# Performance work log

Hardware: AMD Instinct MI355X
Metric: run time of the kernel (lower is better)

Reference implementation:

```python
import jax, jax.numpy as jnp
import numpy as np


def setup_inputs() -> dict:
    key = jax.random.key(0)
    ks = jax.random.split(key, 7)
    B, T, E, H = 4, 4096, 1024, 64
    return {
        "idx": jax.random.normal(ks[0], (B, T, E), dtype=jnp.float32),
        "Wq": jax.random.normal(ks[1], (E, H), dtype=jnp.float32) * (E ** -0.5),
        "bq": jax.random.normal(ks[2], (H,), dtype=jnp.float32) * 0.01,
        "Wk": jax.random.normal(ks[3], (E, H), dtype=jnp.float32) * (E ** -0.5),
        "bk": jax.random.normal(ks[4], (H,), dtype=jnp.float32) * 0.01,
        "Wv": jax.random.normal(ks[5], (E, H), dtype=jnp.float32) * (E ** -0.5),
        "bv": jax.random.normal(ks[6], (H,), dtype=jnp.float32) * 0.01,
    }


def reference(idx, Wq, bq, Wk, bk, Wv, bv):
    # idx: [B, T, E]
    d = idx.shape[-1]  # note: torch code scales by n_embd**-0.5, NOT head_size
    Q = idx @ Wq + bq  # [B, T, H]
    K = idx @ Wk + bk
    V = idx @ Wv + bv
    # scores; NOTE: original torch code calls wei.masked_fill(...) non-in-place
    # and discards the result, so no causal mask is applied. No softmax either.
    wei = jnp.einsum("bth,bsh->bts", Q, K) * (d ** -0.5)  # [B, T, T]
    out = jnp.einsum("bts,bsh->bth", wei, V)  # [B, T, H]
    return out
```

## Files before the change

kernel.cpp:

```cpp
#include <hip/hip_runtime.h>


typedef __attribute__((ext_vector_type(8))) short bf16x8;
typedef __attribute__((ext_vector_type(4))) float f32x4;

#define MFMA16(a, b, c) __builtin_amdgcn_mfma_f32_16x16x32_bf16((a), (b), (c), 0, 0, 0)

__device__ __forceinline__ unsigned short f2bf(float f) {
    unsigned int u = __float_as_uint(f);
    u += 0x7fffu + ((u >> 16) & 1u);
    return (unsigned short)(u >> 16);
}

__global__ void prep(const float* __restrict__ Wq, const float* __restrict__ Wk,
                     const float* __restrict__ Wv, unsigned short* __restrict__ WB) {
    int t = blockIdx.x * 256 + threadIdx.x;
    int kki = t / 768;
    int rem = t - kki * 768;
    int nt = rem >> 6, lane = rem & 63;
    int n = nt * 16 + (lane & 15);
    int kb = kki * 32 + ((lane >> 4) * 8);
    int mm = n >> 6, h = n & 63;
    const float* W = (mm == 0) ? Wq : (mm == 1) ? Wk : Wv;
    float sc = (mm == 1) ? 0.03125f : 1.0f;
    bf16x8 v;
    #pragma unroll
    for (int j = 0; j < 8; j++) v[j] = (short)f2bf(W[(size_t)(kb + j) * 64 + h] * sc);
    *(bf16x8*)(WB + (size_t)t * 8) = v;
}

__global__ __launch_bounds__(256, 4) void qkv(
    const float* __restrict__ idx, const unsigned short* __restrict__ WB,
    const float* __restrict__ bq, const float* __restrict__ bk, const float* __restrict__ bv,
    unsigned short* __restrict__ Q, unsigned short* __restrict__ Kt,
    unsigned short* __restrict__ Vt) {
    __shared__ unsigned short As[16 * 1032];
    const int lane = threadIdx.x & 63, w = threadIdx.x >> 6;
    const int r0 = blockIdx.x * 16;

    const float* src = idx + (size_t)(r0 + w * 4) * 1024;
    #pragma unroll
    for (int batch = 0; batch < 2; batch++) {
        float4 v[8];
        #pragma unroll
        for (int j = 0; j < 8; j++)
            v[j] = *(const float4*)(src + (size_t)(batch * 8 + j) * 256 + lane * 4);
        #pragma unroll
        for (int j = 0; j < 8; j++) {
            int i   = batch * 8 + j;
            int row = w * 4 + (i >> 2);
            int k   = (i & 3) * 256 + lane * 4;
            unsigned int lo = ((unsigned int)f2bf(v[j].y) << 16) | f2bf(v[j].x);
            unsigned int hi = ((unsigned int)f2bf(v[j].w) << 16) | f2bf(v[j].z);
            uint2 p; p.x = lo; p.y = hi;
            *(uint2*)(As + (size_t)row * 1032 + k) = p;
        }
    }
    __syncthreads();

    const f32x4 z4 = {0.f, 0.f, 0.f, 0.f};
    f32x4 acc[3] = {z4, z4, z4};

    const unsigned short* a_base = As + (size_t)(lane & 15) * 1032 + ((lane >> 4) * 8);
    bf16x8 a_c = *(const bf16x8*)(a_base);
    bf16x8 bc[3], bn[3];
    {
        const unsigned short* Bp = WB + (size_t)(lane * 8);
        #pragma unroll
        for (int j = 0; j < 3; j++) bc[j] = *(const bf16x8*)(Bp + (w + j * 4) * 512);
    }
    for (int kk = 0; kk < 32; kk++) {
        bf16x8 a_n = a_c;
        if (kk < 31) {
            const unsigned short* Bp = WB + (size_t)(((kk + 1) * 12) * 64 + lane) * 8;
            #pragma unroll
            for (int j = 0; j < 3; j++) bn[j] = *(const bf16x8*)(Bp + (w + j * 4) * 512);
            a_n = *(const bf16x8*)(a_base + (kk + 1) * 32);
        }
        #pragma unroll
        for (int j = 0; j < 3; j++) acc[j] = MFMA16(a_c, bc[j], acc[j]);
        #pragma unroll
        for (int j = 0; j < 3; j++) bc[j] = bn[j];
        a_c = a_n;
    }

    __syncthreads();
    unsigned short* Lq = As;
    unsigned short* Lk = As + 1024;
    unsigned short* Lv = As + 2048;
    const int h   = w * 16 + (lane & 15);
    const int row = (lane >> 4) * 4;
    {
        float bias0 = bq[h], bias1 = bk[h] * 0.03125f, bias2 = bv[h];
        #pragma unroll
        for (int reg = 0; reg < 4; reg++) {
            int r = row + reg;
            Lq[r * 64 + h] = f2bf(acc[0][reg] + bias0);
            Lk[h * 16 + r] = f2bf(acc[1][reg] + bias1);
            Lv[h * 16 + r] = f2bf(acc[2][reg] + bias2);
        }
    }
    __syncthreads();
    {
        const int tt = threadIdx.x;
        int qr = tt >> 4, qh = (tt & 15) * 4;
        *(uint2*)(Q + (size_t)(r0 + qr) * 64 + qh) = *(const uint2*)(Lq + qr * 64 + qh);
        int b = r0 >> 12, t0 = r0 & 4095;
        int hh = tt >> 2, tc = (tt & 3) * 4;
        *(uint2*)(Kt + (size_t)b * 262144 + hh * 4096 + t0 + tc) =
            *(const uint2*)(Lk + hh * 16 + tc);
        *(uint2*)(Vt + (size_t)b * 262144 + hh * 4096 + t0 + tc) =
            *(const uint2*)(Lv + hh * 16 + tc);
    }
}

__global__ __launch_bounds__(256) void ktv_partial(
    const unsigned short* __restrict__ Kt, const unsigned short* __restrict__ Vt,
    float* __restrict__ part) {
    const int lane = threadIdx.x & 63, wave = threadIdx.x >> 6;
    const int c = blockIdx.x, b = blockIdx.y;
    const unsigned short* Kb = Kt + (size_t)b * 262144;
    const unsigned short* Vb = Vt + (size_t)b * 262144;
    const f32x4 z4 = {0.f, 0.f, 0.f, 0.f};
    f32x4 acc[4] = {z4, z4, z4, z4};
    const int m  = 16 * wave + (lane & 15);
    const int tq = (lane >> 4) * 8;
    #pragma unroll
    for (int it = 0; it < 4; it++) {
        int t0 = c * 128 + it * 32 + tq;
        bf16x8 a = *(const bf16x8*)&Kb[(size_t)m * 4096 + t0];
        #pragma unroll
        for (int nt = 0; nt < 4; nt++) {
            bf16x8 bb = *(const bf16x8*)&Vb[(size_t)(nt * 16 + (lane & 15)) * 4096 + t0];
            acc[nt] = MFMA16(a, bb, acc[nt]);
        }
    }
    float* P = part + (size_t)(b * 32 + c) * 4096;
    const int rowb = 16 * wave + (lane >> 4) * 4;
    #pragma unroll
    for (int nt = 0; nt < 4; nt++)
        #pragma unroll
        for (int reg = 0; reg < 4; reg++)
            P[(rowb + reg) * 64 + nt * 16 + (lane & 15)] = acc[nt][reg];
}

__global__ void reduce_m(const float* __restrict__ part,
                         unsigned short* __restrict__ Mt) {
    int i = blockIdx.x * 256 + threadIdx.x;
    int b = i >> 12, h1 = (i >> 6) & 63, h2 = i & 63;
    float s = 0.f;
    #pragma unroll
    for (int cc = 0; cc < 32; cc++)
        s += part[(size_t)(b * 32 + cc) * 4096 + h1 * 64 + h2];
    Mt[(size_t)b * 4096 + h2 * 64 + h1] = f2bf(s);
}

__global__ __launch_bounds__(256) void qm(
    const unsigned short* __restrict__ Q, const unsigned short* __restrict__ Mt,
    float* __restrict__ out) {
    const int lane = threadIdx.x & 63, wave = threadIdx.x >> 6;
    const int r0 = blockIdx.x * 64;
    const int b  = r0 >> 12;
    const f32x4 z4 = {0.f, 0.f, 0.f, 0.f};
    f32x4 acc[4] = {z4, z4, z4, z4};
    const int rr = r0 + 16 * wave + (lane & 15);
    const int kq = (lane >> 4) * 8;
    #pragma unroll
    for (int ks = 0; ks < 2; ks++) {
        int k0 = ks * 32;
        bf16x8 a = *(const bf16x8*)&Q[(size_t)rr * 64 + k0 + kq];
        #pragma unroll
        for (int nt = 0; nt < 4; nt++) {
            bf16x8 bb = *(const bf16x8*)&Mt[(size_t)b * 4096 + (nt * 16 + (lane & 15)) * 64 + k0 + kq];
            acc[nt] = MFMA16(a, bb, acc[nt]);
        }
    }
    const int rowb = r0 + 16 * wave + (lane >> 4) * 4;
    #pragma unroll
    for (int nt = 0; nt < 4; nt++)
        #pragma unroll
        for (int reg = 0; reg < 4; reg++)
            out[(size_t)(rowb + reg) * 64 + nt * 16 + (lane & 15)] = acc[nt][reg];
}

extern "C" void kernel_launch(void* const* d_in, const int* in_sizes, int n_in,
                              void* d_out, int out_size, void* d_ws, size_t ws_size,
                              hipStream_t stream) {
    const float* idx = (const float*)d_in[0];
    const float* Wq  = (const float*)d_in[1];
    const float* bq  = (const float*)d_in[2];
    const float* Wk  = (const float*)d_in[3];
    const float* bk  = (const float*)d_in[4];
    const float* Wv  = (const float*)d_in[5];
    const float* bv  = (const float*)d_in[6];
    float* out = (float*)d_out;

    char* ws = (char*)d_ws;
    unsigned short* WB = (unsigned short*)(ws);
    float*          Pp = (float*)(ws);
    unsigned short* Q  = (unsigned short*)(ws + (2048u << 10));
    unsigned short* Kt = (unsigned short*)(ws + (4096u << 10));
    unsigned short* Vt = (unsigned short*)(ws + (6144u << 10));
    unsigned short* Mt = (unsigned short*)(ws + (8192u << 10));

    hipLaunchKernelGGL(prep,        dim3(96),     dim3(256), 0, stream, Wq, Wk, Wv, WB);
    hipLaunchKernelGGL(qkv,         dim3(1024),   dim3(256), 0, stream,
                       idx, WB, bq, bk, bv, Q, Kt, Vt);
    hipLaunchKernelGGL(ktv_partial, dim3(32, 4),  dim3(256), 0, stream, Kt, Vt, Pp);
    hipLaunchKernelGGL(reduce_m,    dim3(64),     dim3(256), 0, stream, Pp, Mt);
    hipLaunchKernelGGL(qm,          dim3(256),    dim3(256), 0, stream, Q, Mt, out);
}
```

Baseline: 125.9 us.

## Double rows per QKV block and fold K^T V reduction into atomics

The QKV projection block now handles 32 rows instead of 16, so each weight fragment loaded from global memory feeds two MFMAs. The B prefetch is also deepened to two steps ahead, and the Q/K/V stores are widened to 16 bytes. The separate reduce kernel is removed: ktv atomically adds its partials into a float M zeroed by prep, and qm converts and transposes M into LDS itself. This saves one launch and the partial-buffer traffic, at the cost of lower occupancy in qkv and atomic contention on the shared M.

```diff
diff --git a/kernel.cpp b/kernel.cpp
--- a/kernel.cpp
+++ b/kernel.cpp
@@ -13,8 +13,10 @@
 }
 
 __global__ void prep(const float* __restrict__ Wq, const float* __restrict__ Wk,
-                     const float* __restrict__ Wv, unsigned short* __restrict__ WB) {
+                     const float* __restrict__ Wv, unsigned short* __restrict__ WB,
+                     float* __restrict__ Mf) {
     int t = blockIdx.x * 256 + threadIdx.x;
+    if (t < 16384) Mf[t] = 0.f;
     int kki = t / 768;
     int rem = t - kki * 768;
     int nt = rem >> 6, lane = rem & 63;
@@ -29,18 +31,18 @@
     *(bf16x8*)(WB + (size_t)t * 8) = v;
 }
 
-__global__ __launch_bounds__(256, 4) void qkv(
+__global__ __launch_bounds__(256, 2) void qkv(
     const float* __restrict__ idx, const unsigned short* __restrict__ WB,
     const float* __restrict__ bq, const float* __restrict__ bk, const float* __restrict__ bv,
     unsigned short* __restrict__ Q, unsigned short* __restrict__ Kt,
     unsigned short* __restrict__ Vt) {
-    __shared__ unsigned short As[16 * 1032];
+    __shared__ unsigned short As[32 * 1032];
     const int lane = threadIdx.x & 63, w = threadIdx.x >> 6;
-    const int r0 = blockIdx.x * 16;
-
-    const float* src = idx + (size_t)(r0 + w * 4) * 1024;
-    #pragma unroll
-    for (int batch = 0; batch < 2; batch++) {
+    const int r0 = blockIdx.x * 32;
+
+    const float* src = idx + (size_t)(r0 + w * 8) * 1024;
+    #pragma unroll
+    for (int batch = 0; batch < 4; batch++) {
         float4 v[8];
         #pragma unroll
         for (int j = 0; j < 8; j++)
@@ -48,7 +50,7 @@
         #pragma unroll
         for (int j = 0; j < 8; j++) {
             int i   = batch * 8 + j;
-            int row = w * 4 + (i >> 2);
+            int row = w * 8 + (i >> 2);
             int k   = (i & 3) * 256 + lane * 4;
             unsigned int lo = ((unsigned int)f2bf(v[j].y) << 16) | f2bf(v[j].x);
             unsigned int hi = ((unsigned int)f2bf(v[j].w) << 16) | f2bf(v[j].z);
@@ -59,64 +61,80 @@
     __syncthreads();
 
     const f32x4 z4 = {0.f, 0.f, 0.f, 0.f};
-    f32x4 acc[3] = {z4, z4, z4};
-
-    const unsigned short* a_base = As + (size_t)(lane & 15) * 1032 + ((lane >> 4) * 8);
-    bf16x8 a_c = *(const bf16x8*)(a_base);
-    bf16x8 bc[3], bn[3];
-    {
-        const unsigned short* Bp = WB + (size_t)(lane * 8);
-        #pragma unroll
-        for (int j = 0; j < 3; j++) bc[j] = *(const bf16x8*)(Bp + (w + j * 4) * 512);
+    f32x4 acc[2][3] = {{z4, z4, z4}, {z4, z4, z4}};
+
+    const unsigned short* a_base0 = As + (size_t)(lane & 15) * 1032 + ((lane >> 4) * 8);
+    const unsigned short* a_base1 = a_base0 + 16 * 1032;
+    bf16x8 a_c[2], b0[3], b1[3], b2[3];
+    a_c[0] = *(const bf16x8*)a_base0;
+    a_c[1] = *(const bf16x8*)a_base1;
+    {
+        const unsigned short* Bp0 = WB + (size_t)(lane * 8);
+        const unsigned short* Bp1 = WB + (size_t)(12 * 64 + lane) * 8;
+        #pragma unroll
+        for (int j = 0; j < 3; j++) {
+            b0[j] = *(const bf16x8*)(Bp0 + (w + j * 4) * 512);
+            b1[j] = *(const bf16x8*)(Bp1 + (w + j * 4) * 512);
+            b2[j] = b1[j];
+        }
     }
     for (int kk = 0; kk < 32; kk++) {
-        bf16x8 a_n = a_c;
+        bf16x8 na0 = a_c[0], na1 = a_c[1];
+        if (kk < 30) {
+            const unsigned short* Bp = WB + (size_t)(((kk + 2) * 12) * 64 + lane) * 8;
+            #pragma unroll
+            for (int j = 0; j < 3; j++) b2[j] = *(const bf16x8*)(Bp + (w + j * 4) * 512);
+        }
         if (kk < 31) {
-            const unsigned short* Bp = WB + (size_t)(((kk + 1) * 12) * 64 + lane) * 8;
+            na0 = *(const bf16x8*)(a_base0 + (kk + 1) * 32);
+            na1 = *(const bf16x8*)(a_base1 + (kk + 1) * 32);
+        }
+        #pragma unroll
+        for (int j = 0; j < 3; j++) {
+            acc[0][j] = MFMA16(a_c[0], b0[j], acc[0][j]);
+            acc[1][j] = MFMA16(a_c[1], b0[j], acc[1][j]);
+        }
+        #pragma unroll
+        for (int j = 0; j < 3; j++) { b0[j] = b1[j]; b1[j] = b2[j]; }
+        a_c[0] = na0; a_c[1] = na1;
+    }
+
+    __syncthreads();
+    unsigned short* Lq = As;
+    unsigned short* Lk = As + 2048;
+    unsigned short* Lv = As + 4096;
+    const int h     = w * 16 + (lane & 15);
+    const int rbase = (lane >> 4) * 4;
+    {
+        float bias0 = bq[h], bias1 = bk[h] * 0.03125f, bias2 = bv[h];
+        #pragma unroll
+        for (int rf = 0; rf < 2; rf++) {
             #pragma unroll
-            for (int j = 0; j < 3; j++) bn[j] = *(const bf16x8*)(Bp + (w + j * 4) * 512);
-            a_n = *(const bf16x8*)(a_base + (kk + 1) * 32);
-        }
-        #pragma unroll
-        for (int j = 0; j < 3; j++) acc[j] = MFMA16(a_c, bc[j], acc[j]);
-        #pragma unroll
-        for (int j = 0; j < 3; j++) bc[j] = bn[j];
-        a_c = a_n;
-    }
-
-    __syncthreads();
-    unsigned short* Lq = As;
-    unsigned short* Lk = As + 1024;
-    unsigned short* Lv = As + 2048;
-    const int h   = w * 16 + (lane & 15);
-    const int row = (lane >> 4) * 4;
-    {
-        float bias0 = bq[h], bias1 = bk[h] * 0.03125f, bias2 = bv[h];
-        #pragma unroll
-        for (int reg = 0; reg < 4; reg++) {
-            int r = row + reg;
-            Lq[r * 64 + h] = f2bf(acc[0][reg] + bias0);
-            Lk[h * 16 + r] = f2bf(acc[1][reg] + bias1);
-            Lv[h * 16 + r] = f2bf(acc[2][reg] + bias2);
+            for (int reg = 0; reg < 4; reg++) {
+                int r = rf * 16 + rbase + reg;
+                Lq[r * 64 + h] = f2bf(acc[rf][0][reg] + bias0);
+                Lk[h * 32 + r] = f2bf(acc[rf][1][reg] + bias1);
+                Lv[h * 32 + r] = f2bf(acc[rf][2][reg] + bias2);
+            }
         }
     }
     __syncthreads();
     {
         const int tt = threadIdx.x;
-        int qr = tt >> 4, qh = (tt & 15) * 4;
-        *(uint2*)(Q + (size_t)(r0 + qr) * 64 + qh) = *(const uint2*)(Lq + qr * 64 + qh);
+        int qr = tt >> 3, qh = (tt & 7) * 8;
+        *(uint4*)(Q + (size_t)(r0 + qr) * 64 + qh) = *(const uint4*)(Lq + qr * 64 + qh);
         int b = r0 >> 12, t0 = r0 & 4095;
-        int hh = tt >> 2, tc = (tt & 3) * 4;
-        *(uint2*)(Kt + (size_t)b * 262144 + hh * 4096 + t0 + tc) =
-            *(const uint2*)(Lk + hh * 16 + tc);
-        *(uint2*)(Vt + (size_t)b * 262144 + hh * 4096 + t0 + tc) =
-            *(const uint2*)(Lv + hh * 16 + tc);
-    }
-}
-
-__global__ __launch_bounds__(256) void ktv_partial(
+        int hh = tt >> 2, tc = (tt & 3) * 8;
+        *(uint4*)(Kt + (size_t)b * 262144 + hh * 4096 + t0 + tc) =
+            *(const uint4*)(Lk + hh * 32 + tc);
+        *(uint4*)(Vt + (size_t)b * 262144 + hh * 4096 + t0 + tc) =
+            *(const uint4*)(Lv + hh * 32 + tc);
+    }
+}
+
+__global__ __launch_bounds__(256) void ktv(
     const unsigned short* __restrict__ Kt, const unsigned short* __restrict__ Vt,
-    float* __restrict__ part) {
+    float* __restrict__ Mf) {
     const int lane = threadIdx.x & 63, wave = threadIdx.x >> 6;
     const int c = blockIdx.x, b = blockIdx.y;
     const unsigned short* Kb = Kt + (size_t)b * 262144;
@@ -135,32 +153,35 @@
             acc[nt] = MFMA16(a, bb, acc[nt]);
         }
     }
-    float* P = part + (size_t)(b * 32 + c) * 4096;
+    float* P = Mf + (size_t)b * 4096;
     const int rowb = 16 * wave + (lane >> 4) * 4;
     #pragma unroll
     for (int nt = 0; nt < 4; nt++)
         #pragma unroll
         for (int reg = 0; reg < 4; reg++)
-            P[(rowb + reg) * 64 + nt * 16 + (lane & 15)] = acc[nt][reg];
-}
-
-__global__ void reduce_m(const float* __restrict__ part,
-                         unsigned short* __restrict__ Mt) {
-    int i = blockIdx.x * 256 + threadIdx.x;
-    int b = i >> 12, h1 = (i >> 6) & 63, h2 = i & 63;
-    float s = 0.f;
-    #pragma unroll
-    for (int cc = 0; cc < 32; cc++)
-        s += part[(size_t)(b * 32 + cc) * 4096 + h1 * 64 + h2];
-    Mt[(size_t)b * 4096 + h2 * 64 + h1] = f2bf(s);
+            atomicAdd(&P[(rowb + reg) * 64 + nt * 16 + (lane & 15)], acc[nt][reg]);
 }
 
 __global__ __launch_bounds__(256) void qm(
-    const unsigned short* __restrict__ Q, const unsigned short* __restrict__ Mt,
+    const unsigned short* __restrict__ Q, const float* __restrict__ Mf,
     float* __restrict__ out) {
+    __shared__ unsigned short Lm[64 * 72];
     const int lane = threadIdx.x & 63, wave = threadIdx.x >> 6;
     const int r0 = blockIdx.x * 64;
     const int b  = r0 >> 12;
+    {
+        const int tt = threadIdx.x;
+        int h1 = tt >> 2, h2c = (tt & 3) * 16;
+        const float* Mp = Mf + (size_t)b * 4096 + h1 * 64 + h2c;
+        float vals[16];
+        *(float4*)(vals + 0)  = *(const float4*)(Mp + 0);
+        *(float4*)(vals + 4)  = *(const float4*)(Mp + 4);
+        *(float4*)(vals + 8)  = *(const float4*)(Mp + 8);
+        *(float4*)(vals + 12) = *(const float4*)(Mp + 12);
+        #pragma unroll
+        for (int u = 0; u < 16; u++) Lm[(h2c + u) * 72 + h1] = f2bf(vals[u]);
+    }
+    __syncthreads();
     const f32x4 z4 = {0.f, 0.f, 0.f, 0.f};
     f32x4 acc[4] = {z4, z4, z4, z4};
     const int rr = r0 + 16 * wave + (lane & 15);
@@ -171,7 +192,7 @@
         bf16x8 a = *(const bf16x8*)&Q[(size_t)rr * 64 + k0 + kq];
         #pragma unroll
         for (int nt = 0; nt < 4; nt++) {
-            bf16x8 bb = *(const bf16x8*)&Mt[(size_t)b * 4096 + (nt * 16 + (lane & 15)) * 64 + k0 + kq];
+            bf16x8 bb = *(const bf16x8*)&Lm[(size_t)(nt * 16 + (lane & 15)) * 72 + k0 + kq];
             acc[nt] = MFMA16(a, bb, acc[nt]);
         }
     }
@@ -197,16 +218,14 @@
 
     char* ws = (char*)d_ws;
     unsigned short* WB = (unsigned short*)(ws);
-    float*          Pp = (float*)(ws);
+    float*          Mf = (float*)(ws + (1024u << 10));
     unsigned short* Q  = (unsigned short*)(ws + (2048u << 10));
     unsigned short* Kt = (unsigned short*)(ws + (4096u << 10));
     unsigned short* Vt = (unsigned short*)(ws + (6144u << 10));
-    unsigned short* Mt = (unsigned short*)(ws + (8192u << 10));
-
-    hipLaunchKernelGGL(prep,        dim3(96),     dim3(256), 0, stream, Wq, Wk, Wv, WB);
-    hipLaunchKernelGGL(qkv,         dim3(1024),   dim3(256), 0, stream,
+
+    hipLaunchKernelGGL(prep, dim3(96),    dim3(256), 0, stream, Wq, Wk, Wv, WB, Mf);
+    hipLaunchKernelGGL(qkv,  dim3(512),   dim3(256), 0, stream,
                        idx, WB, bq, bk, bv, Q, Kt, Vt);
-    hipLaunchKernelGGL(ktv_partial, dim3(32, 4),  dim3(256), 0, stream, Kt, Vt, Pp);
-    hipLaunchKernelGGL(reduce_m,    dim3(64),     dim3(256), 0, stream, Pp, Mt);
-    hipLaunchKernelGGL(qm,          dim3(256),    dim3(256), 0, stream, Q, Mt, out);
-}
+    hipLaunchKernelGGL(ktv,  dim3(32, 4), dim3(256), 0, stream, Kt, Vt, Mf);
+    hipLaunchKernelGGL(qm,   dim3(256),   dim3(256), 0, stream, Q, Mf, out);
+}
```

Result: faster. 121.9 us (-3.2%).
